# Kernel optimization log

Hardware: AMD Instinct MI355X
Metric: run time of the kernel (lower is better)

Reference implementation:

```python
import jax, jax.numpy as jnp
import numpy as np

B, L, D = 16384, 32, 128
DIAG_LEN, PROC_LEN, MED_LEN = 100000, 50000, 1000


def setup_inputs() -> dict:
    key = jax.random.key(0)
    ks = jax.random.split(key, 12)
    inp = {
        "diag_codes": jax.random.randint(ks[0], (B, L), 0, DIAG_LEN),
        "proc_codes": jax.random.randint(ks[1], (B, L), 0, PROC_LEN),
        "prev_diag_codes": jax.random.randint(ks[2], (B, L), 0, DIAG_LEN),
        "prev_proc_codes": jax.random.randint(ks[3], (B, L), 0, PROC_LEN),
        # learned parameters (torch Linear convention: W[out,in], y = x @ W.T + b)
        "diag_emb": jax.random.normal(ks[4], (DIAG_LEN, D), jnp.float32) * 0.02,
        "proc_emb": jax.random.normal(ks[5], (PROC_LEN, D), jnp.float32) * 0.02,
        "W1": jax.random.normal(ks[6], (D, 2 * D), jnp.float32) * 0.02,
        "b1": jnp.zeros((D,), jnp.float32),
        "W2": jax.random.normal(ks[7], (256, 2 * D), jnp.float32) * 0.02,
        "b2": jnp.zeros((256,), jnp.float32),
        "W3": jax.random.normal(ks[8], (MED_LEN, 256), jnp.float32) * 0.02,
        "b3": jnp.zeros((MED_LEN,), jnp.float32),
    }
    return inp


def _bag_sum(table, idx):
    # EmbeddingBag('sum'): gather [B,L,D] then reduce over codes -> [B,D]
    return jnp.take(table, idx, axis=0).sum(axis=1)


def reference(diag_codes, proc_codes, prev_diag_codes, prev_proc_codes,
              diag_emb, proc_emb, W1, b1, W2, b2, W3, b3):
    emb_d = _bag_sum(diag_emb, diag_codes)            # [B,128]
    emb_p = _bag_sum(proc_emb, proc_codes)            # [B,128]
    prev_d = _bag_sum(diag_emb, prev_diag_codes)      # [B,128]
    prev_p = _bag_sum(proc_emb, prev_proc_codes)      # [B,128]

    # health_net = Linear(256->128) + Dropout (identity in eval mode)
    cur = jnp.concatenate([emb_d, emb_p], axis=1) @ W1.T + b1     # [B,128]
    prev = jnp.concatenate([prev_d, prev_p], axis=1) @ W1.T + b1  # [B,128]

    rep = jnp.concatenate([cur, prev], axis=1)        # [B,256]
    h = jax.nn.relu(rep @ W2.T + b2)                  # [B,256]
    return jax.nn.sigmoid(h @ W3.T + b3)              # [B,med_len]
```

## Files before the change

### kernel.cpp

```cpp
#include <hip/hip_runtime.h>
#include <hip/hip_bf16.h>
#include <math.h>

#define NB 16384
#define MED 1000
#define MD 100000
#define MP 50000
#define TDBLK 782
#define TPBLK 391

typedef __bf16 bf16x8 __attribute__((ext_vector_type(8)));
typedef float  f32x4  __attribute__((ext_vector_type(4)));
typedef unsigned short u16;
typedef unsigned int   u32;

__device__ __forceinline__ u16 f2bf(float f) {
    union { float f; u32 u; } v; v.f = f;
    u32 r = v.u + 0x7fffu + ((v.u >> 16) & 1u);
    return (u16)(r >> 16);
}
__device__ __forceinline__ float bflo(u32 u) { union { u32 u; float f; } v; v.u = u << 16;          return v.f; }
__device__ __forceinline__ float bfhi(u32 u) { union { u32 u; float f; } v; v.u = u & 0xffff0000u; return v.f; }

__global__ __launch_bounds__(256) void convert_kernel(
    const float* __restrict__ W1, const float* __restrict__ W2,
    const float* __restrict__ W3,
    u16* __restrict__ W1b, u16* __restrict__ W2b, u16* __restrict__ W3b)
{
    int i = blockIdx.x * 256 + threadIdx.x;
    if (i < 32768) { W1b[i] = f2bf(W1[i]); return; }
    i -= 32768;
    if (i < 65536) { W2b[i] = f2bf(W2[i]); return; }
    i -= 65536;
    if (i < 262144) W3b[i] = (i < MED * 256) ? f2bf(W3[i]) : (u16)0;
}

__global__ __launch_bounds__(256) void transform_kernel(
    const float* __restrict__ Ed, const float* __restrict__ Ep,
    const u16* __restrict__ W1b, u16* __restrict__ Td, u16* __restrict__ Tp)
{
    int blk = blockIdx.x;
    const float* E; u16* T; int M, koff;
    if (blk < TDBLK) { E = Ed; T = Td; M = MD; koff = 0; }
    else             { blk -= TDBLK; E = Ep; T = Tp; M = MP; koff = 128; }

    const int wave = threadIdx.x >> 6, lane = threadIdx.x & 63;
    const int quad = lane >> 4, l16 = lane & 15;
    const int m0 = blk * 128 + wave * 32 + l16;
    const float* aP0 = E + (size_t)min(m0,      M - 1) * 128 + quad * 8;
    const float* aP1 = E + (size_t)min(m0 + 16, M - 1) * 128 + quad * 8;
    const u16*   wP  = W1b + (size_t)l16 * 256 + koff + quad * 8;

    f32x4 acc[2][8];
    #pragma unroll
    for (int mt = 0; mt < 2; ++mt)
        #pragma unroll
        for (int nt = 0; nt < 8; ++nt) acc[mt][nt] = (f32x4){0.f, 0.f, 0.f, 0.f};

    #pragma unroll
    for (int ks = 0; ks < 4; ++ks) {
        union { bf16x8 v; u16 s[8]; } a0, a1;
        const float4 f0 = *(const float4*)(aP0 + ks * 32);
        const float4 f1 = *(const float4*)(aP0 + ks * 32 + 4);
        const float4 g0 = *(const float4*)(aP1 + ks * 32);
        const float4 g1 = *(const float4*)(aP1 + ks * 32 + 4);
        a0.s[0]=f2bf(f0.x); a0.s[1]=f2bf(f0.y); a0.s[2]=f2bf(f0.z); a0.s[3]=f2bf(f0.w);
        a0.s[4]=f2bf(f1.x); a0.s[5]=f2bf(f1.y); a0.s[6]=f2bf(f1.z); a0.s[7]=f2bf(f1.w);
        a1.s[0]=f2bf(g0.x); a1.s[1]=f2bf(g0.y); a1.s[2]=f2bf(g0.z); a1.s[3]=f2bf(g0.w);
        a1.s[4]=f2bf(g1.x); a1.s[5]=f2bf(g1.y); a1.s[6]=f2bf(g1.z); a1.s[7]=f2bf(g1.w);
        #pragma unroll
        for (int nt = 0; nt < 8; ++nt) {
            const bf16x8 b = *(const bf16x8*)(wP + nt * 16 * 256 + ks * 32);
            acc[0][nt] = __builtin_amdgcn_mfma_f32_16x16x32_bf16(a0.v, b, acc[0][nt], 0, 0, 0);
            acc[1][nt] = __builtin_amdgcn_mfma_f32_16x16x32_bf16(a1.v, b, acc[1][nt], 0, 0, 0);
        }
    }

    #pragma unroll
    for (int mt = 0; mt < 2; ++mt) {
        const int rb = blk * 128 + wave * 32 + mt * 16 + quad * 4;
        #pragma unroll
        for (int nt = 0; nt < 8; ++nt) {
            const int col = nt * 16 + l16;
            #pragma unroll
            for (int r = 0; r < 4; ++r) {
                const int row = rb + r;
                if (row < M) T[(size_t)row * 128 + col] = f2bf(acc[mt][nt][r]);
            }
        }
    }
}

__global__ __launch_bounds__(256) void gather_rep(
    const int* __restrict__ diag, const int* __restrict__ proc,
    const int* __restrict__ pdiag, const int* __restrict__ pproc,
    const u16* __restrict__ Td, const u16* __restrict__ Tp,
    const float* __restrict__ b1, u16* __restrict__ rep)
{
    __shared__ int   sidx[528];
    __shared__ float sred[128][8];
    const int t = threadIdx.x;

    for (int i = t; i < 512; i += 256) {
        const int s = i >> 7, bg = (i >> 5) & 3, l = i & 31;
        const int* cp = (bg == 0) ? diag : (bg == 1) ? proc : (bg == 2) ? pdiag : pproc;
        sidx[s * 132 + bg * 33 + l] = cp[(blockIdx.x * 4 + s) * 32 + l];
    }
    __syncthreads();

    const int sub = t >> 6, bag = (t >> 4) & 3, lc = t & 15;
    const u16* tbl = (bag & 1) ? Tp : Td;
    const int* myidx = &sidx[sub * 132 + bag * 33];

    float s0=0,s1=0,s2=0,s3=0,s4=0,s5=0,s6=0,s7=0;
    #pragma unroll
    for (int g = 0; g < 4; ++g) {
        uint4 v[8];
        #pragma unroll
        for (int j = 0; j < 8; ++j)
            v[j] = *(const uint4*)(tbl + (size_t)myidx[g * 8 + j] * 128 + lc * 8);
        #pragma unroll
        for (int j = 0; j < 8; ++j) {
            s0 += bflo(v[j].x); s1 += bfhi(v[j].x);
            s2 += bflo(v[j].y); s3 += bfhi(v[j].y);
            s4 += bflo(v[j].z); s5 += bfhi(v[j].z);
            s6 += bflo(v[j].w); s7 += bfhi(v[j].w);
        }
    }

    const int oid = sub * 32 + (bag >> 1) * 16 + lc;
    if (bag & 1) {
        *(float4*)&sred[oid][0] = make_float4(s0, s1, s2, s3);
        *(float4*)&sred[oid][4] = make_float4(s4, s5, s6, s7);
    }
    __syncthreads();
    if (!(bag & 1)) {
        const float4 p0 = *(const float4*)&sred[oid][0];
        const float4 p1 = *(const float4*)&sred[oid][4];
        const float4 c0 = *(const float4*)(b1 + lc * 8);
        const float4 c1 = *(const float4*)(b1 + lc * 8 + 4);
        s0 += p0.x + c0.x; s1 += p0.y + c0.y; s2 += p0.z + c0.z; s3 += p0.w + c0.w;
        s4 += p1.x + c1.x; s5 += p1.y + c1.y; s6 += p1.z + c1.z; s7 += p1.w + c1.w;
        uint4 o;
        o.x = (u32)f2bf(s0) | ((u32)f2bf(s1) << 16);
        o.y = (u32)f2bf(s2) | ((u32)f2bf(s3) << 16);
        o.z = (u32)f2bf(s4) | ((u32)f2bf(s5) << 16);
        o.w = (u32)f2bf(s6) | ((u32)f2bf(s7) << 16);
        const int b = blockIdx.x * 4 + sub;
        *(uint4*)(rep + (size_t)b * 256 + (bag >> 1) * 128 + lc * 8) = o;
    }
}

template<int EPI>
__global__ __launch_bounds__(256) void gemm_bt(
    const u16* __restrict__ A, const u16* __restrict__ W,
    const float* __restrict__ bias, void* __restrict__ outp)
{
    const int wave = threadIdx.x >> 6, lane = threadIdx.x & 63;
    const int quad = lane >> 4, l16 = lane & 15;
    const int mBase = blockIdx.x * 128 + wave * 32;
    const int nBase = blockIdx.y * 64;
    const u16* aP0 = A + (size_t)(mBase + l16) * 256 + quad * 8;
    const u16* aP1 = aP0 + 16 * 256;
    const u16* wP  = W + (size_t)(nBase + l16) * 256 + quad * 8;

    f32x4 acc[2][4];
    #pragma unroll
    for (int mt = 0; mt < 2; ++mt)
        #pragma unroll
        for (int nt = 0; nt < 4; ++nt) acc[mt][nt] = (f32x4){0.f, 0.f, 0.f, 0.f};

    #pragma unroll
    for (int ks = 0; ks < 8; ++ks) {
        const bf16x8 a0 = *(const bf16x8*)(aP0 + ks * 32);
        const bf16x8 a1 = *(const bf16x8*)(aP1 + ks * 32);
        #pragma unroll
        for (int nt = 0; nt < 4; ++nt) {
            const bf16x8 b = *(const bf16x8*)(wP + nt * 16 * 256 + ks * 32);
            acc[0][nt] = __builtin_amdgcn_mfma_f32_16x16x32_bf16(a0, b, acc[0][nt], 0, 0, 0);
            acc[1][nt] = __builtin_amdgcn_mfma_f32_16x16x32_bf16(a1, b, acc[1][nt], 0, 0, 0);
        }
    }

    #pragma unroll
    for (int mt = 0; mt < 2; ++mt) {
        const int rowB = mBase + mt * 16 + quad * 4;
        #pragma unroll
        for (int nt = 0; nt < 4; ++nt) {
            const int col = nBase + nt * 16 + l16;
            if (EPI == 2) {
                if (col < MED) {
                    const float bv = bias[col];
                    float* out = (float*)outp;
                    #pragma unroll
                    for (int r = 0; r < 4; ++r) {
                        const float v = acc[mt][nt][r] + bv;
                        out[(size_t)(rowB + r) * MED + col] = 1.0f / (1.0f + __expf(-v));
                    }
                }
            } else {
                const float bv = bias[col];
                u16* out = (u16*)outp;
                #pragma unroll
                for (int r = 0; r < 4; ++r) {
                    float v = acc[mt][nt][r] + bv;
                    v = v > 0.f ? v : 0.f;
                    out[(size_t)(rowB + r) * 256 + col] = f2bf(v);
                }
            }
        }
    }
}

extern "C" void kernel_launch(void* const* d_in, const int* in_sizes, int n_in,
                              void* d_out, int out_size, void* d_ws, size_t ws_size,
                              hipStream_t stream)
{
    const int*   diag  = (const int*)d_in[0];
    const int*   proc  = (const int*)d_in[1];
    const int*   pdiag = (const int*)d_in[2];
    const int*   pproc = (const int*)d_in[3];
    const float* demb  = (const float*)d_in[4];
    const float* pemb  = (const float*)d_in[5];
    const float* W1    = (const float*)d_in[6];
    const float* b1    = (const float*)d_in[7];
    const float* W2    = (const float*)d_in[8];
    const float* b2    = (const float*)d_in[9];
    const float* W3    = (const float*)d_in[10];
    const float* b3    = (const float*)d_in[11];

    char* ws = (char*)d_ws;
    u16* Td  = (u16*)ws;
    u16* Tp  = (u16*)(ws + 25600000);
    u16* rep = (u16*)(ws + 38400000);
    u16* W1b = (u16*)(ws + 46788608);
    u16* W2b = (u16*)(ws + 46854144);
    u16* W3b = (u16*)(ws + 46985216);
    u16* h   = (u16*)ws;

    convert_kernel<<<1408, 256, 0, stream>>>(W1, W2, W3, W1b, W2b, W3b);
    transform_kernel<<<TDBLK + TPBLK, 256, 0, stream>>>(demb, pemb, W1b, Td, Tp);
    gather_rep<<<NB / 4, 256, 0, stream>>>(diag, proc, pdiag, pproc, Td, Tp, b1, rep);
    gemm_bt<1><<<dim3(128, 4), 256, 0, stream>>>(rep, W2b, b2, h);
    gemm_bt<2><<<dim3(128, 16), 256, 0, stream>>>(h, W3b, b3, d_out);
}
```

Baseline: 300.0 us.

## Fuse second and third GEMMs via shared-memory hidden tile; pipeline gather loads

Merges the W2 and W3 GEMMs into one kernel. Each block computes a 32-row hidden tile with ReLU, stores it in LDS as bf16, then multiplies it by W3 to produce the sigmoid output, so the hidden activations no longer make a round trip through global memory and one launch is dropped. The gather kernel is also restructured to keep two batches of table loads in flight while summing the previous batch. In exchange, W2 and W3 are reread from L2 by all 512 blocks, each block does more serial work, and register pressure is higher.

```diff
diff --git a/kernel.cpp b/kernel.cpp
--- a/kernel.cpp
+++ b/kernel.cpp
@@ -113,20 +113,44 @@
     const int* myidx = &sidx[sub * 132 + bag * 33];
 
     float s0=0,s1=0,s2=0,s3=0,s4=0,s5=0,s6=0,s7=0;
-    #pragma unroll
-    for (int g = 0; g < 4; ++g) {
-        uint4 v[8];
+    uint4 va[8], vb[8];
+    #pragma unroll
+    for (int j = 0; j < 8; ++j)
+        va[j] = *(const uint4*)(tbl + (size_t)myidx[j] * 128 + lc * 8);
+    #pragma unroll
+    for (int j = 0; j < 8; ++j)
+        vb[j] = *(const uint4*)(tbl + (size_t)myidx[8 + j] * 128 + lc * 8);
+
+#define CONSUME(V) do { \
+    _Pragma("unroll") \
+    for (int j = 0; j < 8; ++j) { \
+        s0 += bflo(V[j].x); s1 += bfhi(V[j].x); \
+        s2 += bflo(V[j].y); s3 += bfhi(V[j].y); \
+        s4 += bflo(V[j].z); s5 += bfhi(V[j].z); \
+        s6 += bflo(V[j].w); s7 += bfhi(V[j].w); \
+    } } while (0)
+
+    {
+        uint4 tmp[8];
         #pragma unroll
         for (int j = 0; j < 8; ++j)
-            v[j] = *(const uint4*)(tbl + (size_t)myidx[g * 8 + j] * 128 + lc * 8);
-        #pragma unroll
-        for (int j = 0; j < 8; ++j) {
-            s0 += bflo(v[j].x); s1 += bfhi(v[j].x);
-            s2 += bflo(v[j].y); s3 += bfhi(v[j].y);
-            s4 += bflo(v[j].z); s5 += bfhi(v[j].z);
-            s6 += bflo(v[j].w); s7 += bfhi(v[j].w);
-        }
-    }
+            tmp[j] = *(const uint4*)(tbl + (size_t)myidx[16 + j] * 128 + lc * 8);
+        CONSUME(va);
+        #pragma unroll
+        for (int j = 0; j < 8; ++j) va[j] = tmp[j];
+    }
+    {
+        uint4 tmp[8];
+        #pragma unroll
+        for (int j = 0; j < 8; ++j)
+            tmp[j] = *(const uint4*)(tbl + (size_t)myidx[24 + j] * 128 + lc * 8);
+        CONSUME(vb);
+        #pragma unroll
+        for (int j = 0; j < 8; ++j) vb[j] = tmp[j];
+    }
+    CONSUME(va);
+    CONSUME(vb);
+#undef CONSUME
 
     const int oid = sub * 32 + (bag >> 1) * 16 + lc;
     if (bag & 1) {
@@ -151,61 +175,81 @@
     }
 }
 
-template<int EPI>
-__global__ __launch_bounds__(256) void gemm_bt(
-    const u16* __restrict__ A, const u16* __restrict__ W,
-    const float* __restrict__ bias, void* __restrict__ outp)
-{
+__global__ __launch_bounds__(256) void gemm23(
+    const u16* __restrict__ rep, const u16* __restrict__ W2b,
+    const float* __restrict__ b2, const u16* __restrict__ W3b,
+    const float* __restrict__ b3, float* __restrict__ out)
+{
+    __shared__ u16 hs[32][264];
     const int wave = threadIdx.x >> 6, lane = threadIdx.x & 63;
     const int quad = lane >> 4, l16 = lane & 15;
-    const int mBase = blockIdx.x * 128 + wave * 32;
-    const int nBase = blockIdx.y * 64;
-    const u16* aP0 = A + (size_t)(mBase + l16) * 256 + quad * 8;
-    const u16* aP1 = aP0 + 16 * 256;
-    const u16* wP  = W + (size_t)(nBase + l16) * 256 + quad * 8;
-
-    f32x4 acc[2][4];
-    #pragma unroll
-    for (int mt = 0; mt < 2; ++mt)
-        #pragma unroll
-        for (int nt = 0; nt < 4; ++nt) acc[mt][nt] = (f32x4){0.f, 0.f, 0.f, 0.f};
-
-    #pragma unroll
-    for (int ks = 0; ks < 8; ++ks) {
-        const bf16x8 a0 = *(const bf16x8*)(aP0 + ks * 32);
-        const bf16x8 a1 = *(const bf16x8*)(aP1 + ks * 32);
-        #pragma unroll
-        for (int nt = 0; nt < 4; ++nt) {
-            const bf16x8 b = *(const bf16x8*)(wP + nt * 16 * 256 + ks * 32);
-            acc[0][nt] = __builtin_amdgcn_mfma_f32_16x16x32_bf16(a0, b, acc[0][nt], 0, 0, 0);
-            acc[1][nt] = __builtin_amdgcn_mfma_f32_16x16x32_bf16(a1, b, acc[1][nt], 0, 0, 0);
-        }
-    }
-
-    #pragma unroll
-    for (int mt = 0; mt < 2; ++mt) {
-        const int rowB = mBase + mt * 16 + quad * 4;
-        #pragma unroll
-        for (int nt = 0; nt < 4; ++nt) {
-            const int col = nBase + nt * 16 + l16;
-            if (EPI == 2) {
-                if (col < MED) {
-                    const float bv = bias[col];
-                    float* out = (float*)outp;
+    const int mBase = blockIdx.x * 32;
+
+    {
+        const int mrow = mBase + (wave & 1) * 16 + l16;
+        const int ncol0 = (wave >> 1) * 128;
+        const u16* aP = rep + (size_t)mrow * 256 + quad * 8;
+        bf16x8 a[8];
+        #pragma unroll
+        for (int ks = 0; ks < 8; ++ks) a[ks] = *(const bf16x8*)(aP + ks * 32);
+
+        #pragma unroll
+        for (int nt = 0; nt < 8; ++nt) {
+            const int col = ncol0 + nt * 16 + l16;
+            const u16* wP = W2b + (size_t)col * 256 + quad * 8;
+            f32x4 acc = {0.f, 0.f, 0.f, 0.f};
+            #pragma unroll
+            for (int ks = 0; ks < 8; ++ks) {
+                const bf16x8 b = *(const bf16x8*)(wP + ks * 32);
+                acc = __builtin_amdgcn_mfma_f32_16x16x32_bf16(a[ks], b, acc, 0, 0, 0);
+            }
+            const float bv = b2[col];
+            #pragma unroll
+            for (int r = 0; r < 4; ++r) {
+                float v = acc[r] + bv;
+                v = v > 0.f ? v : 0.f;
+                hs[(wave & 1) * 16 + quad * 4 + r][col] = f2bf(v);
+            }
+        }
+    }
+    __syncthreads();
+
+    const int colW = wave * 256;
+    #pragma unroll
+    for (int nc = 0; nc < 4; ++nc) {
+        f32x4 acc[2][4];
+        #pragma unroll
+        for (int mt = 0; mt < 2; ++mt)
+            #pragma unroll
+            for (int nti = 0; nti < 4; ++nti) acc[mt][nti] = (f32x4){0.f,0.f,0.f,0.f};
+
+        #pragma unroll
+        for (int ks = 0; ks < 8; ++ks) {
+            bf16x8 af[2];
+            #pragma unroll
+            for (int mt = 0; mt < 2; ++mt)
+                af[mt] = *(const bf16x8*)&hs[mt * 16 + l16][quad * 8 + ks * 32];
+            #pragma unroll
+            for (int nti = 0; nti < 4; ++nti) {
+                const int wrow = colW + nc * 64 + nti * 16 + l16;
+                const bf16x8 b = *(const bf16x8*)(W3b + (size_t)wrow * 256 + quad * 8 + ks * 32);
+                acc[0][nti] = __builtin_amdgcn_mfma_f32_16x16x32_bf16(af[0], b, acc[0][nti], 0, 0, 0);
+                acc[1][nti] = __builtin_amdgcn_mfma_f32_16x16x32_bf16(af[1], b, acc[1][nti], 0, 0, 0);
+            }
+        }
+        #pragma unroll
+        for (int nti = 0; nti < 4; ++nti) {
+            const int col = colW + nc * 64 + nti * 16 + l16;
+            if (col < MED) {
+                const float bv = b3[col];
+                #pragma unroll
+                for (int mt = 0; mt < 2; ++mt) {
                     #pragma unroll
                     for (int r = 0; r < 4; ++r) {
-                        const float v = acc[mt][nt][r] + bv;
-                        out[(size_t)(rowB + r) * MED + col] = 1.0f / (1.0f + __expf(-v));
+                        const float v = acc[mt][nti][r] + bv;
+                        out[(size_t)(mBase + mt * 16 + quad * 4 + r) * MED + col] =
+                            1.0f / (1.0f + __expf(-v));
                     }
-                }
-            } else {
-                const float bv = bias[col];
-                u16* out = (u16*)outp;
-                #pragma unroll
-                for (int r = 0; r < 4; ++r) {
-                    float v = acc[mt][nt][r] + bv;
-                    v = v > 0.f ? v : 0.f;
-                    out[(size_t)(rowB + r) * 256 + col] = f2bf(v);
                 }
             }
         }
@@ -236,11 +280,9 @@
     u16* W1b = (u16*)(ws + 46788608);
     u16* W2b = (u16*)(ws + 46854144);
     u16* W3b = (u16*)(ws + 46985216);
-    u16* h   = (u16*)ws;
 
     convert_kernel<<<1408, 256, 0, stream>>>(W1, W2, W3, W1b, W2b, W3b);
     transform_kernel<<<TDBLK + TPBLK, 256, 0, stream>>>(demb, pemb, W1b, Td, Tp);
     gather_rep<<<NB / 4, 256, 0, stream>>>(diag, proc, pdiag, pproc, Td, Tp, b1, rep);
-    gemm_bt<1><<<dim3(128, 4), 256, 0, stream>>>(rep, W2b, b2, h);
-    gemm_bt<2><<<dim3(128, 16), 256, 0, stream>>>(h, W3b, b3, d_out);
-}
+    gemm23<<<512, 256, 0, stream>>>(rep, W2b, b2, W3b, b3, (float*)d_out);
+}
```

Measured after the change: 293.6 us. 1.02x faster.
